# Optimization experiments

Hardware: AMD Instinct MI355X
Metric: run time of the kernel (lower is better)

Reference implementation:

```python
import jax, jax.numpy as jnp
import numpy as np

GE = 8            # graph_embedding_size
AGG_MEAN = 0.0    # undefined global in source; dataset statistic, fixed here
AGG_VAR = 1.0
N_NODES = 100000
N_EDGES = 3200000


def setup_inputs() -> dict:
    key = jax.random.key(0)
    ks = jax.random.split(key, 17)

    def w(k, shape):
        fan_in = shape[0]
        return jax.random.normal(k, shape, jnp.float32) / np.float32(np.sqrt(fan_in))

    x = jax.random.normal(ks[0], (N_NODES, 1 + GE), jnp.float32)
    edge_attr = jax.random.uniform(ks[1], (N_EDGES, 1), dtype=jnp.float32)
    edge_index = jax.random.randint(ks[2], (2, N_EDGES), 0, N_NODES, dtype=jnp.int32)

    # mlp1: Lin(9,32)+ReLU, Lin(32,32)+ReLU, Lin(32,1)+Sigmoid
    W1, b1 = w(ks[3], (1 + GE, 32)), jnp.zeros((32,), jnp.float32)
    W2, b2 = w(ks[4], (32, 32)), jnp.zeros((32,), jnp.float32)
    W3, b3 = w(ks[5], (32, 1)), jnp.zeros((1,), jnp.float32)
    # mlp2: Lin(10,16)+ReLU, Lin(16,8)+ReLU
    V1, c1 = w(ks[6], (2 + GE, 16)), jnp.zeros((16,), jnp.float32)
    V2, c2 = w(ks[7], (16, GE)), jnp.zeros((GE,), jnp.float32)
    # h2o: Lin(8,16)+ReLU, Lin(16,1)+Sigmoid
    H1, d1 = w(ks[8], (GE, 16)), jnp.zeros((16,), jnp.float32)
    H2, d2 = w(ks[9], (16, 1)), jnp.zeros((1,), jnp.float32)

    return {"x": x, "edge_attr": edge_attr, "edge_index": edge_index,
            "W1": W1, "b1": b1, "W2": W2, "b2": b2, "W3": W3, "b3": b3,
            "V1": V1, "c1": c1, "V2": V2, "c2": c2,
            "H1": H1, "d1": d1, "H2": H2, "d2": d2}


def reference(x, edge_attr, edge_index, W1, b1, W2, b2, W3, b3,
              V1, c1, V2, c2, H1, d1, H2, d2):
    src = edge_index[0]  # x_j gathered from source nodes (PyG default flow)
    dst = edge_index[1]  # aggregate into target nodes
    n = x.shape[0]

    def air_conv(xc):
        xj = xc[src]                                            # [E, 9] gather
        h = jax.nn.relu(xj @ W1 + b1)                           # [E, 32]
        h = jax.nn.relu(h @ W2 + b2)                            # [E, 32]
        msg = jax.nn.sigmoid(h @ W3 + b3) * edge_attr           # [E, 1]
        agg = jax.ops.segment_sum(msg, dst, num_segments=n)     # [N, 1] scatter-add
        norm = (agg - AGG_MEAN) / AGG_VAR
        t = jnp.concatenate([xc, norm], axis=1)                 # [N, 10]
        comb = jax.nn.relu(jax.nn.relu(t @ V1 + c1) @ V2 + c2)  # [N, 8]
        return jnp.concatenate([xc[:, :1], comb], axis=1)       # [N, 9]

    out = air_conv(air_conv(air_conv(x)))
    h = jax.nn.relu(out[:, 1:] @ H1 + d1)                       # [N, 16]
    return jax.nn.sigmoid(h @ H2 + d2)                          # [N, 1]
```

## Files before the change

kernel.cpp:

```cpp
#include <hip/hip_runtime.h>

typedef unsigned int uint;
typedef unsigned char uchar;


#define NPB 512
#define NPB_SHIFT 9
#define MAXB 256
#define NBLK 640
#define AGG_THREADS 512

__device__ __forceinline__ void load_smem(float* dstp, const float* __restrict__ srcp,
                                          int n, int tid, int nthreads) {
    for (int i = tid; i < n; i += nthreads) dstp[i] = srcp[i];
}

__device__ __forceinline__ float mlp1_eval(const float* xj,
    const float* sW1, const float* sb1, const float* sW2, const float* sb2,
    const float* sW3, float sb3)
{
    float h1[32];
#pragma unroll
    for (int j = 0; j < 32; ++j) h1[j] = sb1[j];
#pragma unroll
    for (int i = 0; i < 9; ++i) {
        float v = xj[i];
#pragma unroll
        for (int j = 0; j < 32; ++j) h1[j] = fmaf(v, sW1[i*32+j], h1[j]);
    }
#pragma unroll
    for (int j = 0; j < 32; ++j) h1[j] = fmaxf(h1[j], 0.0f);
    float h2[32];
#pragma unroll
    for (int j = 0; j < 32; ++j) h2[j] = sb2[j];
#pragma unroll
    for (int i = 0; i < 32; ++i) {
        float v = h1[i];
#pragma unroll
        for (int j = 0; j < 32; ++j) h2[j] = fmaf(v, sW2[i*32+j], h2[j]);
    }
    float m = sb3;
#pragma unroll
    for (int i = 0; i < 32; ++i) m = fmaf(fmaxf(h2[i], 0.0f), sW3[i], m);
    return 1.0f / (1.0f + __expf(-m));
}

__global__ __launch_bounds__(256) void p0_kernel(
    const float* __restrict__ x,
    const float* __restrict__ W1, const float* __restrict__ b1,
    const float* __restrict__ W2, const float* __restrict__ b2,
    const float* __restrict__ W3, const float* __restrict__ b3,
    float* __restrict__ p, float* __restrict__ agg3, int N)
{
    __shared__ float sW1[288], sb1[32], sW2[1024], sb2[32], sW3[32], sb3s[1];
    int tid = threadIdx.x;
    load_smem(sW1, W1, 288, tid, 256);
    load_smem(sb1, b1, 32, tid, 256);
    load_smem(sW2, W2, 1024, tid, 256);
    load_smem(sb2, b2, 32, tid, 256);
    load_smem(sW3, W3, 32, tid, 256);
    if (tid == 0) sb3s[0] = b3[0];
    __syncthreads();
    int n = blockIdx.x * 256 + tid;
    if (n >= N) return;
    if (agg3) { agg3[n] = 0.0f; agg3[N + n] = 0.0f; agg3[2*(size_t)N + n] = 0.0f; }
    float xj[9];
#pragma unroll
    for (int i = 0; i < 9; ++i) xj[i] = x[(size_t)n*9 + i];
    p[n] = mlp1_eval(xj, sW1, sb1, sW2, sb2, sW3, sb3s[0]);
}


__global__ __launch_bounds__(256) void hist_kernel(
    const int* __restrict__ dst, uint* __restrict__ hist_g, int E, int chunk, int B)
{
    __shared__ uint hist[MAXB];
    int tid = threadIdx.x;
    for (int i = tid; i < MAXB; i += 256) hist[i] = 0u;
    __syncthreads();
    int start = blockIdx.x * chunk;
    int end = min(E, start + chunk);
    for (int e = start + tid; e < end; e += 256)
        atomicAdd(&hist[((uint)dst[e]) >> NPB_SHIFT], 1u);
    __syncthreads();
    for (int b = tid; b < B; b += 256)
        hist_g[(size_t)b * NBLK + blockIdx.x] = hist[b];
}

__global__ __launch_bounds__(1024) void scanA_kernel(
    uint* __restrict__ hist_g, uint* __restrict__ total)
{
    __shared__ uint s[1024];
    int t = threadIdx.x;
    int b = blockIdx.x;
    uint v = (t < NBLK) ? hist_g[(size_t)b * NBLK + t] : 0u;
    s[t] = v;
    __syncthreads();
    for (int off = 1; off < 1024; off <<= 1) {
        uint xv = (t >= off) ? s[t - off] : 0u;
        __syncthreads();
        s[t] += xv;
        __syncthreads();
    }
    if (t < NBLK) hist_g[(size_t)b * NBLK + t] = s[t] - v;
    if (t == NBLK - 1) total[b] = s[t];
}

__global__ __launch_bounds__(1024) void scanB_kernel(
    const uint* __restrict__ total, uint* __restrict__ base, int B)
{
    __shared__ uint s[1024];
    int t = threadIdx.x;
    uint v = (t < B) ? total[t] : 0u;
    s[t] = v;
    __syncthreads();
    for (int off = 1; off < 1024; off <<= 1) {
        uint xv = (t >= off) ? s[t - off] : 0u;
        __syncthreads();
        s[t] += xv;
        __syncthreads();
    }
    if (t < B) base[t] = s[t] - v;
    if (t == B - 1) base[B] = s[t];
}

__global__ __launch_bounds__(256) void scatter_sort_kernel(
    const int* __restrict__ dst, const int* __restrict__ src,
    const float* __restrict__ ea, const uint* __restrict__ base,
    const uint* __restrict__ hist_g,
    int2* __restrict__ ia, int E, int chunk, int B)
{
    __shared__ uint cnt[MAXB];
    int tid = threadIdx.x;
    for (int b = tid; b < B; b += 256)
        cnt[b] = base[b] + hist_g[(size_t)b * NBLK + blockIdx.x];
    __syncthreads();
    int start = blockIdx.x * chunk;
    int end = min(E, start + chunk);
    for (int e = start + tid; e < end; e += 256) {
        uint d = (uint)dst[e];
        uint bin = d >> NPB_SHIFT;
        uint pos = atomicAdd(&cnt[bin], 1u);
        int2 v;
        v.x = (int)(((uint)src[e] << NPB_SHIFT) | (d & (NPB - 1)));
        v.y = __float_as_int(ea[e]);
        ia[pos] = v;
    }
}

template<bool LAST>
__global__ __launch_bounds__(AGG_THREADS) void aggnode_kernel(
    const float* __restrict__ xin,
    const int2* __restrict__ ia,
    const uint* __restrict__ base, const float* __restrict__ p_in,
    const float* __restrict__ V1, const float* __restrict__ c1,
    const float* __restrict__ V2, const float* __restrict__ c2,
    const float* __restrict__ W1, const float* __restrict__ b1,
    const float* __restrict__ W2, const float* __restrict__ b2,
    const float* __restrict__ W3, const float* __restrict__ b3,
    const float* __restrict__ H1, const float* __restrict__ d1,
    const float* __restrict__ H2, const float* __restrict__ d2,
    float* __restrict__ xout, float* __restrict__ pout,
    float* __restrict__ finalout, int N)
{
    __shared__ float aggl[NPB];
    __shared__ float sV1[160], sc1[16], sV2[128], sc2[8];
    __shared__ float sW1[288], sb1[32], sW2[1024], sb2[32], sW3[32], sbx[1];
    __shared__ float sH1[128], sd1[16], sH2[16], sdx[1];
    int tid = threadIdx.x;
    for (int i = tid; i < NPB; i += AGG_THREADS) aggl[i] = 0.0f;
    load_smem(sV1, V1, 160, tid, AGG_THREADS);
    load_smem(sc1, c1, 16, tid, AGG_THREADS);
    load_smem(sV2, V2, 128, tid, AGG_THREADS);
    load_smem(sc2, c2, 8, tid, AGG_THREADS);
    if (!LAST) {
        load_smem(sW1, W1, 288, tid, AGG_THREADS);
        load_smem(sb1, b1, 32, tid, AGG_THREADS);
        load_smem(sW2, W2, 1024, tid, AGG_THREADS);
        load_smem(sb2, b2, 32, tid, AGG_THREADS);
        load_smem(sW3, W3, 32, tid, AGG_THREADS);
        if (tid == 0) sbx[0] = b3[0];
    } else {
        load_smem(sH1, H1, 128, tid, AGG_THREADS);
        load_smem(sd1, d1, 16, tid, AGG_THREADS);
        load_smem(sH2, H2, 16, tid, AGG_THREADS);
        if (tid == 0) sdx[0] = d2[0];
    }
    __syncthreads();

    int b = blockIdx.x;
    uint e0 = base[b], e1 = base[b + 1];
    for (uint e = e0 + tid; e < e1; e += AGG_THREADS) {
        int2 v = ia[e];
        float pv = p_in[(uint)v.x >> NPB_SHIFT];
        atomicAdd(&aggl[(uint)v.x & (NPB - 1)], pv * __int_as_float(v.y));
    }
    __syncthreads();

    int n = b * NPB + tid;
    if (tid >= NPB || n >= N) return;

    float t[10];
#pragma unroll
    for (int i = 0; i < 9; ++i) t[i] = xin[(size_t)n*9 + i];
    t[9] = aggl[tid];

    float u[16];
#pragma unroll
    for (int j = 0; j < 16; ++j) u[j] = sc1[j];
#pragma unroll
    for (int i = 0; i < 10; ++i) {
        float v = t[i];
#pragma unroll
        for (int j = 0; j < 16; ++j) u[j] = fmaf(v, sV1[i*16+j], u[j]);
    }
#pragma unroll
    for (int j = 0; j < 16; ++j) u[j] = fmaxf(u[j], 0.0f);

    float comb[8];
#pragma unroll
    for (int j = 0; j < 8; ++j) comb[j] = sc2[j];
#pragma unroll
    for (int i = 0; i < 16; ++i) {
        float v = u[i];
#pragma unroll
        for (int j = 0; j < 8; ++j) comb[j] = fmaf(v, sV2[i*8+j], comb[j]);
    }
#pragma unroll
    for (int j = 0; j < 8; ++j) comb[j] = fmaxf(comb[j], 0.0f);

    if (!LAST) {
        float xnew[9];
        xnew[0] = t[0];
#pragma unroll
        for (int j = 0; j < 8; ++j) xnew[1+j] = comb[j];
#pragma unroll
        for (int i = 0; i < 9; ++i) xout[(size_t)n*9 + i] = xnew[i];
        pout[n] = mlp1_eval(xnew, sW1, sb1, sW2, sb2, sW3, sbx[0]);
    } else {
        float hh[16];
#pragma unroll
        for (int j = 0; j < 16; ++j) hh[j] = sd1[j];
#pragma unroll
        for (int i = 0; i < 8; ++i) {
            float v = comb[i];
#pragma unroll
            for (int j = 0; j < 16; ++j) hh[j] = fmaf(v, sH1[i*16+j], hh[j]);
        }
        float o = sdx[0];
#pragma unroll
        for (int j = 0; j < 16; ++j) o = fmaf(fmaxf(hh[j], 0.0f), sH2[j], o);
        finalout[n] = 1.0f / (1.0f + __expf(-o));
    }
}


__global__ __launch_bounds__(256) void scatter_kernel4(
    const float* __restrict__ p, const int* __restrict__ src, const int* __restrict__ dst,
    const float* __restrict__ eattr, float* __restrict__ agg, int E)
{
    int i = (blockIdx.x * 256 + threadIdx.x) * 4;
    if (i + 3 < E) {
        int4   s = *(const int4*)(src + i);
        int4   d = *(const int4*)(dst + i);
        float4 a = *(const float4*)(eattr + i);
        atomicAdd(&agg[d.x], p[s.x] * a.x);
        atomicAdd(&agg[d.y], p[s.y] * a.y);
        atomicAdd(&agg[d.z], p[s.z] * a.z);
        atomicAdd(&agg[d.w], p[s.w] * a.w);
    } else {
        for (; i < E; ++i) atomicAdd(&agg[dst[i]], p[src[i]] * eattr[i]);
    }
}

template<bool LAST>
__global__ __launch_bounds__(256) void node_kernel(
    const float* __restrict__ xin, const float* __restrict__ agg,
    const float* __restrict__ V1, const float* __restrict__ c1,
    const float* __restrict__ V2, const float* __restrict__ c2,
    const float* __restrict__ W1, const float* __restrict__ b1,
    const float* __restrict__ W2, const float* __restrict__ b2,
    const float* __restrict__ W3, const float* __restrict__ b3,
    const float* __restrict__ H1, const float* __restrict__ d1,
    const float* __restrict__ H2, const float* __restrict__ d2,
    float* __restrict__ xout, float* __restrict__ pout,
    float* __restrict__ finalout, int N)
{
    __shared__ float sV1[160], sc1[16], sV2[128], sc2[8];
    __shared__ float sW1[288], sb1[32], sW2[1024], sb2[32], sW3[32], sbx[1];
    __shared__ float sH1[128], sd1[16], sH2[16], sdx[1];
    int tid = threadIdx.x;
    load_smem(sV1, V1, 160, tid, 256);
    load_smem(sc1, c1, 16, tid, 256);
    load_smem(sV2, V2, 128, tid, 256);
    load_smem(sc2, c2, 8, tid, 256);
    if (!LAST) {
        load_smem(sW1, W1, 288, tid, 256);
        load_smem(sb1, b1, 32, tid, 256);
        load_smem(sW2, W2, 1024, tid, 256);
        load_smem(sb2, b2, 32, tid, 256);
        load_smem(sW3, W3, 32, tid, 256);
        if (tid == 0) sbx[0] = b3[0];
    } else {
        load_smem(sH1, H1, 128, tid, 256);
        load_smem(sd1, d1, 16, tid, 256);
        load_smem(sH2, H2, 16, tid, 256);
        if (tid == 0) sdx[0] = d2[0];
    }
    __syncthreads();
    int n = blockIdx.x * 256 + tid;
    if (n >= N) return;

    float t[10];
#pragma unroll
    for (int i = 0; i < 9; ++i) t[i] = xin[(size_t)n*9 + i];
    t[9] = agg[n];

    float u[16];
#pragma unroll
    for (int j = 0; j < 16; ++j) u[j] = sc1[j];
#pragma unroll
    for (int i = 0; i < 10; ++i) {
        float v = t[i];
#pragma unroll
        for (int j = 0; j < 16; ++j) u[j] = fmaf(v, sV1[i*16+j], u[j]);
    }
#pragma unroll
    for (int j = 0; j < 16; ++j) u[j] = fmaxf(u[j], 0.0f);

    float comb[8];
#pragma unroll
    for (int j = 0; j < 8; ++j) comb[j] = sc2[j];
#pragma unroll
    for (int i = 0; i < 16; ++i) {
        float v = u[i];
#pragma unroll
        for (int j = 0; j < 8; ++j) comb[j] = fmaf(v, sV2[i*8+j], comb[j]);
    }
#pragma unroll
    for (int j = 0; j < 8; ++j) comb[j] = fmaxf(comb[j], 0.0f);

    if (!LAST) {
        float xnew[9];
        xnew[0] = t[0];
#pragma unroll
        for (int j = 0; j < 8; ++j) xnew[1+j] = comb[j];
#pragma unroll
        for (int i = 0; i < 9; ++i) xout[(size_t)n*9 + i] = xnew[i];
        pout[n] = mlp1_eval(xnew, sW1, sb1, sW2, sb2, sW3, sbx[0]);
    } else {
        float hh[16];
#pragma unroll
        for (int j = 0; j < 16; ++j) hh[j] = sd1[j];
#pragma unroll
        for (int i = 0; i < 8; ++i) {
            float v = comb[i];
#pragma unroll
            for (int j = 0; j < 16; ++j) hh[j] = fmaf(v, sH1[i*16+j], hh[j]);
        }
        float o = sdx[0];
#pragma unroll
        for (int j = 0; j < 16; ++j) o = fmaf(fmaxf(hh[j], 0.0f), sH2[j], o);
        finalout[n] = 1.0f / (1.0f + __expf(-o));
    }
}

extern "C" void kernel_launch(void* const* d_in, const int* in_sizes, int n_in,
                              void* d_out, int out_size, void* d_ws, size_t ws_size,
                              hipStream_t stream)
{
    const float* x     = (const float*)d_in[0];
    const float* eattr = (const float*)d_in[1];
    const int*   eidx  = (const int*)d_in[2];
    const float *W1=(const float*)d_in[3],  *b1=(const float*)d_in[4];
    const float *W2=(const float*)d_in[5],  *b2=(const float*)d_in[6];
    const float *W3=(const float*)d_in[7],  *b3=(const float*)d_in[8];
    const float *V1=(const float*)d_in[9],  *c1=(const float*)d_in[10];
    const float *V2=(const float*)d_in[11], *c2=(const float*)d_in[12];
    const float *H1=(const float*)d_in[13], *d1=(const float*)d_in[14];
    const float *H2=(const float*)d_in[15], *d2=(const float*)d_in[16];
    int N = in_sizes[0] / 9;
    int E = in_sizes[1];
    const int* src = eidx;
    const int* dst = eidx + E;
    float* out = (float*)d_out;
    int B = (N + NPB - 1) / NPB;

    size_t need = (size_t)E * 8
                + (size_t)N * 9 * 4 * 2
                + (size_t)N * 4 * 2
                + (size_t)MAXB * NBLK * 4
                + (size_t)MAXB * 4
                + (size_t)(MAXB + 1) * 4
                + 64;

    dim3 thr(256);
    dim3 blkN((N + 255) / 256);

    bool packable = ((long long)N << NPB_SHIFT) < (1LL << 32);

    if (B <= MAXB && packable && ws_size >= need) {
        char* w = (char*)d_ws;
        int2* ia      = (int2*)w;              w += (size_t)E * 8;
        float* xcA    = (float*)w;             w += (size_t)N * 9 * 4;
        float* xcB    = (float*)w;             w += (size_t)N * 9 * 4;
        float* pA     = (float*)w;             w += (size_t)N * 4;
        float* pB     = (float*)w;             w += (size_t)N * 4;
        uint* hist_g  = (uint*)w;              w += (size_t)MAXB * NBLK * 4;
        uint* total   = (uint*)w;              w += (size_t)MAXB * 4;
        uint* base    = (uint*)w;

        int chunk = (E + NBLK - 1) / NBLK;

        p0_kernel<<<blkN, thr, 0, stream>>>(x, W1,b1,W2,b2,W3,b3, pA, nullptr, N);
        hist_kernel<<<dim3(NBLK), thr, 0, stream>>>(dst, hist_g, E, chunk, B);
        scanA_kernel<<<dim3(B), dim3(1024), 0, stream>>>(hist_g, total);
        scanB_kernel<<<dim3(1), dim3(1024), 0, stream>>>(total, base, B);
        scatter_sort_kernel<<<dim3(NBLK), thr, 0, stream>>>(dst, src, eattr, base, hist_g,
                                                            ia, E, chunk, B);
        aggnode_kernel<false><<<dim3(B), dim3(AGG_THREADS), 0, stream>>>(x, ia, base, pA,
            V1,c1,V2,c2, W1,b1,W2,b2,W3,b3, H1,d1,H2,d2, xcA, pB, nullptr, N);
        aggnode_kernel<false><<<dim3(B), dim3(AGG_THREADS), 0, stream>>>(xcA, ia, base, pB,
            V1,c1,V2,c2, W1,b1,W2,b2,W3,b3, H1,d1,H2,d2, xcB, pA, nullptr, N);
        aggnode_kernel<true><<<dim3(B), dim3(AGG_THREADS), 0, stream>>>(xcB, ia, base, pA,
            V1,c1,V2,c2, W1,b1,W2,b2,W3,b3, H1,d1,H2,d2, nullptr, nullptr, out, N);
    } else {
        float* ws   = (float*)d_ws;
        float* xcA  = ws;
        float* xcB  = xcA + (size_t)N * 9;
        float* p    = xcB + (size_t)N * 9;
        float* agg3 = p + N;
        dim3 blkE4(((E + 3) / 4 + 255) / 256);

        p0_kernel<<<blkN, thr, 0, stream>>>(x, W1,b1,W2,b2,W3,b3, p, agg3, N);
        scatter_kernel4<<<blkE4, thr, 0, stream>>>(p, src, dst, eattr, agg3, E);
        node_kernel<false><<<blkN, thr, 0, stream>>>(x, agg3, V1,c1,V2,c2, W1,b1,W2,b2,W3,b3,
                                                     H1,d1,H2,d2, xcA, p, nullptr, N);
        scatter_kernel4<<<blkE4, thr, 0, stream>>>(p, src, dst, eattr, agg3 + N, E);
        node_kernel<false><<<blkN, thr, 0, stream>>>(xcA, agg3 + N, V1,c1,V2,c2, W1,b1,W2,b2,W3,b3,
                                                     H1,d1,H2,d2, xcB, p, nullptr, N);
        scatter_kernel4<<<blkE4, thr, 0, stream>>>(p, src, dst, eattr, agg3 + 2*(size_t)N, E);
        node_kernel<true><<<blkN, thr, 0, stream>>>(xcB, agg3 + 2*(size_t)N, V1,c1,V2,c2,
                                                    W1,b1,W2,b2,W3,b3, H1,d1,H2,d2,
                                                    nullptr, nullptr, out, N);
    }
}
```

Before: 163.4 us.

## Split edge aggregation across sub-blocks and rebuild bucket sort with local partitioning

Aggregation is separated from the node MLP. Each 512-node bucket is now processed by four blocks that write partial sums, which a separate node kernel adds up; this spreads work across far more blocks than the roughly 196 used before. The per-block histogram and two-level scan are replaced by global atomic bucket counts and a single small scan. The scatter sort becomes a shared-memory local partition per 4096-edge chunk, so global writes are more coalesced. In exchange there are extra kernel launches, a partial-sum buffer round trip, and the node features are updated in place in a buffer marked restrict.

```diff
diff --git a/kernel.cpp b/kernel.cpp
--- a/kernel.cpp
+++ b/kernel.cpp
@@ -1,14 +1,16 @@
 #include <hip/hip_runtime.h>
 
 typedef unsigned int uint;
+typedef unsigned short ushort;
 typedef unsigned char uchar;
 
 
 #define NPB 512
 #define NPB_SHIFT 9
 #define MAXB 256
-#define NBLK 640
-#define AGG_THREADS 512
+#define CHUNK 4096
+#define S_SPLIT 4
+#define NBLK_H 640
 
 __device__ __forceinline__ void load_smem(float* dstp, const float* __restrict__ srcp,
                                           int n, int tid, int nthreads) {
@@ -50,7 +52,7 @@
     const float* __restrict__ W1, const float* __restrict__ b1,
     const float* __restrict__ W2, const float* __restrict__ b2,
     const float* __restrict__ W3, const float* __restrict__ b3,
-    float* __restrict__ p, float* __restrict__ agg3, int N)
+    float* __restrict__ p, uint* __restrict__ count, float* __restrict__ agg3, int N)
 {
     __shared__ float sW1[288], sb1[32], sW2[1024], sb2[32], sW3[32], sb3s[1];
     int tid = threadIdx.x;
@@ -61,6 +63,7 @@
     load_smem(sW3, W3, 32, tid, 256);
     if (tid == 0) sb3s[0] = b3[0];
     __syncthreads();
+    if (count && blockIdx.x == 0) count[tid] = 0u;
     int n = blockIdx.x * 256 + tid;
     if (n >= N) return;
     if (agg3) { agg3[n] = 0.0f; agg3[N + n] = 0.0f; agg3[2*(size_t)N + n] = 0.0f; }
@@ -70,89 +73,129 @@
     p[n] = mlp1_eval(xj, sW1, sb1, sW2, sb2, sW3, sb3s[0]);
 }
 
-
-__global__ __launch_bounds__(256) void hist_kernel(
-    const int* __restrict__ dst, uint* __restrict__ hist_g, int E, int chunk, int B)
+__global__ __launch_bounds__(256) void hist_kernel2(
+    const int* __restrict__ dst, uint* __restrict__ count, int E, int B)
 {
     __shared__ uint hist[MAXB];
     int tid = threadIdx.x;
     for (int i = tid; i < MAXB; i += 256) hist[i] = 0u;
     __syncthreads();
-    int start = blockIdx.x * chunk;
-    int end = min(E, start + chunk);
-    for (int e = start + tid; e < end; e += 256)
+    int total = gridDim.x * 256;
+    int gid = blockIdx.x * 256 + tid;
+    int E4 = E >> 2;
+    const int4* dst4 = (const int4*)dst;
+    for (int i = gid; i < E4; i += total) {
+        int4 d = dst4[i];
+        atomicAdd(&hist[((uint)d.x) >> NPB_SHIFT], 1u);
+        atomicAdd(&hist[((uint)d.y) >> NPB_SHIFT], 1u);
+        atomicAdd(&hist[((uint)d.z) >> NPB_SHIFT], 1u);
+        atomicAdd(&hist[((uint)d.w) >> NPB_SHIFT], 1u);
+    }
+    for (int e = 4*E4 + gid; e < E; e += total)
         atomicAdd(&hist[((uint)dst[e]) >> NPB_SHIFT], 1u);
     __syncthreads();
     for (int b = tid; b < B; b += 256)
-        hist_g[(size_t)b * NBLK + blockIdx.x] = hist[b];
-}
-
-__global__ __launch_bounds__(1024) void scanA_kernel(
-    uint* __restrict__ hist_g, uint* __restrict__ total)
-{
-    __shared__ uint s[1024];
+        if (hist[b]) atomicAdd(&count[b], hist[b]);
+}
+
+__global__ __launch_bounds__(256) void scan_kernel(
+    const uint* __restrict__ count, uint* __restrict__ base,
+    uint* __restrict__ cursor, int B)
+{
+    __shared__ uint s[MAXB];
     int t = threadIdx.x;
-    int b = blockIdx.x;
-    uint v = (t < NBLK) ? hist_g[(size_t)b * NBLK + t] : 0u;
+    uint v = (t < B) ? count[t] : 0u;
     s[t] = v;
     __syncthreads();
-    for (int off = 1; off < 1024; off <<= 1) {
+    for (int off = 1; off < MAXB; off <<= 1) {
         uint xv = (t >= off) ? s[t - off] : 0u;
         __syncthreads();
         s[t] += xv;
         __syncthreads();
     }
-    if (t < NBLK) hist_g[(size_t)b * NBLK + t] = s[t] - v;
-    if (t == NBLK - 1) total[b] = s[t];
-}
-
-__global__ __launch_bounds__(1024) void scanB_kernel(
-    const uint* __restrict__ total, uint* __restrict__ base, int B)
-{
-    __shared__ uint s[1024];
-    int t = threadIdx.x;
-    uint v = (t < B) ? total[t] : 0u;
-    s[t] = v;
-    __syncthreads();
-    for (int off = 1; off < 1024; off <<= 1) {
-        uint xv = (t >= off) ? s[t - off] : 0u;
+    uint excl = s[t] - v;
+    if (t < B) { base[t] = excl; cursor[t] = excl; }
+    if (t == B - 1) base[B] = s[t];
+}
+
+__global__ __launch_bounds__(256) void partition_kernel(
+    const int* __restrict__ dst, const int* __restrict__ src,
+    const float* __restrict__ ea, uint* __restrict__ cursor,
+    int2* __restrict__ ia, int E, int B)
+{
+    __shared__ uint hist[MAXB];
+    __shared__ uint off[MAXB];
+    __shared__ uint gbase[MAXB];
+    __shared__ uchar  sbinA[CHUNK];
+    __shared__ ushort sdloc[CHUNK];
+    __shared__ int2  payload[CHUNK];
+    __shared__ uchar sbin[CHUNK];
+    int tid = threadIdx.x;
+    int start = blockIdx.x * CHUNK;
+    int n = min(E - start, CHUNK);
+    for (int i = tid; i < MAXB; i += 256) hist[i] = 0u;
+    __syncthreads();
+    for (int i = tid; i < n; i += 256) {
+        uint d = (uint)dst[start + i];
+        uint b = d >> NPB_SHIFT;
+        sbinA[i] = (uchar)b;
+        sdloc[i] = (ushort)(d & (NPB - 1));
+        atomicAdd(&hist[b], 1u);
+    }
+    __syncthreads();
+    off[tid] = hist[tid];
+    __syncthreads();
+    for (int o = 1; o < MAXB; o <<= 1) {
+        uint xv = (tid >= o) ? off[tid - o] : 0u;
         __syncthreads();
-        s[t] += xv;
+        off[tid] += xv;
         __syncthreads();
     }
-    if (t < B) base[t] = s[t] - v;
-    if (t == B - 1) base[B] = s[t];
-}
-
-__global__ __launch_bounds__(256) void scatter_sort_kernel(
-    const int* __restrict__ dst, const int* __restrict__ src,
-    const float* __restrict__ ea, const uint* __restrict__ base,
-    const uint* __restrict__ hist_g,
-    int2* __restrict__ ia, int E, int chunk, int B)
-{
-    __shared__ uint cnt[MAXB];
-    int tid = threadIdx.x;
-    for (int b = tid; b < B; b += 256)
-        cnt[b] = base[b] + hist_g[(size_t)b * NBLK + blockIdx.x];
-    __syncthreads();
-    int start = blockIdx.x * chunk;
-    int end = min(E, start + chunk);
-    for (int e = start + tid; e < end; e += 256) {
-        uint d = (uint)dst[e];
-        uint bin = d >> NPB_SHIFT;
-        uint pos = atomicAdd(&cnt[bin], 1u);
+    uint cnt_b = hist[tid];
+    uint excl  = off[tid] - cnt_b;
+    gbase[tid] = cnt_b ? atomicAdd(&cursor[tid], cnt_b) : 0u;
+    off[tid]  = excl;
+    hist[tid] = excl;
+    __syncthreads();
+    for (int i = tid; i < n; i += 256) {
+        uint b = sbinA[i];
+        uint s = atomicAdd(&hist[b], 1u);
         int2 v;
-        v.x = (int)(((uint)src[e] << NPB_SHIFT) | (d & (NPB - 1)));
-        v.y = __float_as_int(ea[e]);
-        ia[pos] = v;
-    }
+        v.x = (int)(((uint)src[start + i] << NPB_SHIFT) | (uint)sdloc[i]);
+        v.y = __float_as_int(ea[start + i]);
+        payload[s] = v;
+        sbin[s] = (uchar)b;
+    }
+    __syncthreads();
+    for (int s2 = tid; s2 < n; s2 += 256) {
+        uint b = sbin[s2];
+        ia[gbase[b] + ((uint)s2 - off[b])] = payload[s2];
+    }
+}
+
+__global__ __launch_bounds__(512) void agg_kernel(
+    const int2* __restrict__ ia, const uint* __restrict__ base,
+    const float* __restrict__ p_in, float* __restrict__ aggpart)
+{
+    __shared__ float aggl[NPB];
+    int tid = threadIdx.x;
+    int bkt = blockIdx.x / S_SPLIT;
+    int sub = blockIdx.x % S_SPLIT;
+    aggl[tid] = 0.0f;
+    __syncthreads();
+    uint e0 = base[bkt], e1 = base[bkt + 1];
+    for (uint e = e0 + (uint)sub * 512u + (uint)tid; e < e1; e += S_SPLIT * 512u) {
+        int2 v = ia[e];
+        atomicAdd(&aggl[(uint)v.x & (NPB - 1)],
+                  p_in[(uint)v.x >> NPB_SHIFT] * __int_as_float(v.y));
+    }
+    __syncthreads();
+    aggpart[(size_t)blockIdx.x * NPB + tid] = aggl[tid];
 }
 
 template<bool LAST>
-__global__ __launch_bounds__(AGG_THREADS) void aggnode_kernel(
-    const float* __restrict__ xin,
-    const int2* __restrict__ ia,
-    const uint* __restrict__ base, const float* __restrict__ p_in,
+__global__ __launch_bounds__(512) void node_kernel2(
+    const float* __restrict__ xin, const float* __restrict__ aggpart,
     const float* __restrict__ V1, const float* __restrict__ c1,
     const float* __restrict__ V2, const float* __restrict__ c2,
     const float* __restrict__ W1, const float* __restrict__ b1,
@@ -163,47 +206,42 @@
     float* __restrict__ xout, float* __restrict__ pout,
     float* __restrict__ finalout, int N)
 {
-    __shared__ float aggl[NPB];
     __shared__ float sV1[160], sc1[16], sV2[128], sc2[8];
     __shared__ float sW1[288], sb1[32], sW2[1024], sb2[32], sW3[32], sbx[1];
     __shared__ float sH1[128], sd1[16], sH2[16], sdx[1];
     int tid = threadIdx.x;
-    for (int i = tid; i < NPB; i += AGG_THREADS) aggl[i] = 0.0f;
-    load_smem(sV1, V1, 160, tid, AGG_THREADS);
-    load_smem(sc1, c1, 16, tid, AGG_THREADS);
-    load_smem(sV2, V2, 128, tid, AGG_THREADS);
-    load_smem(sc2, c2, 8, tid, AGG_THREADS);
+    load_smem(sV1, V1, 160, tid, 512);
+    load_smem(sc1, c1, 16, tid, 512);
+    load_smem(sV2, V2, 128, tid, 512);
+    load_smem(sc2, c2, 8, tid, 512);
     if (!LAST) {
-        load_smem(sW1, W1, 288, tid, AGG_THREADS);
-        load_smem(sb1, b1, 32, tid, AGG_THREADS);
-        load_smem(sW2, W2, 1024, tid, AGG_THREADS);
-        load_smem(sb2, b2, 32, tid, AGG_THREADS);
-        load_smem(sW3, W3, 32, tid, AGG_THREADS);
+        load_smem(sW1, W1, 288, tid, 512);
+        load_smem(sb1, b1, 32, tid, 512);
+        load_smem(sW2, W2, 1024, tid, 512);
+        load_smem(sb2, b2, 32, tid, 512);
+        load_smem(sW3, W3, 32, tid, 512);
         if (tid == 0) sbx[0] = b3[0];
     } else {
-        load_smem(sH1, H1, 128, tid, AGG_THREADS);
-        load_smem(sd1, d1, 16, tid, AGG_THREADS);
-        load_smem(sH2, H2, 16, tid, AGG_THREADS);
+        load_smem(sH1, H1, 128, tid, 512);
+        load_smem(sd1, d1, 16, tid, 512);
+        load_smem(sH2, H2, 16, tid, 512);
         if (tid == 0) sdx[0] = d2[0];
     }
     __syncthreads();
 
-    int b = blockIdx.x;
-    uint e0 = base[b], e1 = base[b + 1];
-    for (uint e = e0 + tid; e < e1; e += AGG_THREADS) {
-        int2 v = ia[e];
-        float pv = p_in[(uint)v.x >> NPB_SHIFT];
-        atomicAdd(&aggl[(uint)v.x & (NPB - 1)], pv * __int_as_float(v.y));
-    }
-    __syncthreads();
-
-    int n = b * NPB + tid;
-    if (tid >= NPB || n >= N) return;
+    int bkt = blockIdx.x;
+    int n = bkt * NPB + tid;
+    if (n >= N) return;
+
+    float aggv = 0.0f;
+#pragma unroll
+    for (int s = 0; s < S_SPLIT; ++s)
+        aggv += aggpart[(size_t)(bkt * S_SPLIT + s) * NPB + tid];
 
     float t[10];
 #pragma unroll
     for (int i = 0; i < 9; ++i) t[i] = xin[(size_t)n*9 + i];
-    t[9] = aggl[tid];
+    t[9] = aggv;
 
     float u[16];
 #pragma unroll
@@ -387,42 +425,43 @@
     int B = (N + NPB - 1) / NPB;
 
     size_t need = (size_t)E * 8
-                + (size_t)N * 9 * 4 * 2
+                + (size_t)N * 9 * 4
                 + (size_t)N * 4 * 2
-                + (size_t)MAXB * NBLK * 4
-                + (size_t)MAXB * 4
-                + (size_t)(MAXB + 1) * 4
-                + 64;
-
-    dim3 thr(256);
+                + (size_t)B * S_SPLIT * NPB * 4
+                + (size_t)MAXB * 4 * 3 + 64;
+
+    dim3 thr256(256), thr512(512);
     dim3 blkN((N + 255) / 256);
-
     bool packable = ((long long)N << NPB_SHIFT) < (1LL << 32);
 
     if (B <= MAXB && packable && ws_size >= need) {
         char* w = (char*)d_ws;
-        int2* ia      = (int2*)w;              w += (size_t)E * 8;
-        float* xcA    = (float*)w;             w += (size_t)N * 9 * 4;
-        float* xcB    = (float*)w;             w += (size_t)N * 9 * 4;
-        float* pA     = (float*)w;             w += (size_t)N * 4;
-        float* pB     = (float*)w;             w += (size_t)N * 4;
-        uint* hist_g  = (uint*)w;              w += (size_t)MAXB * NBLK * 4;
-        uint* total   = (uint*)w;              w += (size_t)MAXB * 4;
-        uint* base    = (uint*)w;
-
-        int chunk = (E + NBLK - 1) / NBLK;
-
-        p0_kernel<<<blkN, thr, 0, stream>>>(x, W1,b1,W2,b2,W3,b3, pA, nullptr, N);
-        hist_kernel<<<dim3(NBLK), thr, 0, stream>>>(dst, hist_g, E, chunk, B);
-        scanA_kernel<<<dim3(B), dim3(1024), 0, stream>>>(hist_g, total);
-        scanB_kernel<<<dim3(1), dim3(1024), 0, stream>>>(total, base, B);
-        scatter_sort_kernel<<<dim3(NBLK), thr, 0, stream>>>(dst, src, eattr, base, hist_g,
-                                                            ia, E, chunk, B);
-        aggnode_kernel<false><<<dim3(B), dim3(AGG_THREADS), 0, stream>>>(x, ia, base, pA,
-            V1,c1,V2,c2, W1,b1,W2,b2,W3,b3, H1,d1,H2,d2, xcA, pB, nullptr, N);
-        aggnode_kernel<false><<<dim3(B), dim3(AGG_THREADS), 0, stream>>>(xcA, ia, base, pB,
-            V1,c1,V2,c2, W1,b1,W2,b2,W3,b3, H1,d1,H2,d2, xcB, pA, nullptr, N);
-        aggnode_kernel<true><<<dim3(B), dim3(AGG_THREADS), 0, stream>>>(xcB, ia, base, pA,
+        int2*  ia      = (int2*)w;   w += (size_t)E * 8;
+        float* xc      = (float*)w;  w += (size_t)N * 9 * 4;
+        float* pA      = (float*)w;  w += (size_t)N * 4;
+        float* pB      = (float*)w;  w += (size_t)N * 4;
+        float* aggpart = (float*)w;  w += (size_t)B * S_SPLIT * NPB * 4;
+        uint*  count   = (uint*)w;   w += (size_t)MAXB * 4;
+        uint*  cursor  = (uint*)w;   w += (size_t)MAXB * 4;
+        uint*  base    = (uint*)w;
+
+        dim3 blkP((E + CHUNK - 1) / CHUNK);
+        dim3 blkA(B * S_SPLIT);
+        dim3 blkB(B);
+
+        p0_kernel<<<blkN, thr256, 0, stream>>>(x, W1,b1,W2,b2,W3,b3, pA, count, nullptr, N);
+        hist_kernel2<<<dim3(NBLK_H), thr256, 0, stream>>>(dst, count, E, B);
+        scan_kernel<<<dim3(1), thr256, 0, stream>>>(count, base, cursor, B);
+        partition_kernel<<<blkP, thr256, 0, stream>>>(dst, src, eattr, cursor, ia, E, B);
+
+        agg_kernel<<<blkA, thr512, 0, stream>>>(ia, base, pA, aggpart);
+        node_kernel2<false><<<blkB, thr512, 0, stream>>>(x, aggpart,
+            V1,c1,V2,c2, W1,b1,W2,b2,W3,b3, H1,d1,H2,d2, xc, pB, nullptr, N);
+        agg_kernel<<<blkA, thr512, 0, stream>>>(ia, base, pB, aggpart);
+        node_kernel2<false><<<blkB, thr512, 0, stream>>>(xc, aggpart,
+            V1,c1,V2,c2, W1,b1,W2,b2,W3,b3, H1,d1,H2,d2, xc, pA, nullptr, N);
+        agg_kernel<<<blkA, thr512, 0, stream>>>(ia, base, pA, aggpart);
+        node_kernel2<true><<<blkB, thr512, 0, stream>>>(xc, aggpart,
             V1,c1,V2,c2, W1,b1,W2,b2,W3,b3, H1,d1,H2,d2, nullptr, nullptr, out, N);
     } else {
         float* ws   = (float*)d_ws;
@@ -432,16 +471,16 @@
         float* agg3 = p + N;
         dim3 blkE4(((E + 3) / 4 + 255) / 256);
 
-        p0_kernel<<<blkN, thr, 0, stream>>>(x, W1,b1,W2,b2,W3,b3, p, agg3, N);
-        scatter_kernel4<<<blkE4, thr, 0, stream>>>(p, src, dst, eattr, agg3, E);
-        node_kernel<false><<<blkN, thr, 0, stream>>>(x, agg3, V1,c1,V2,c2, W1,b1,W2,b2,W3,b3,
-                                                     H1,d1,H2,d2, xcA, p, nullptr, N);
-        scatter_kernel4<<<blkE4, thr, 0, stream>>>(p, src, dst, eattr, agg3 + N, E);
-        node_kernel<false><<<blkN, thr, 0, stream>>>(xcA, agg3 + N, V1,c1,V2,c2, W1,b1,W2,b2,W3,b3,
-                                                     H1,d1,H2,d2, xcB, p, nullptr, N);
-        scatter_kernel4<<<blkE4, thr, 0, stream>>>(p, src, dst, eattr, agg3 + 2*(size_t)N, E);
-        node_kernel<true><<<blkN, thr, 0, stream>>>(xcB, agg3 + 2*(size_t)N, V1,c1,V2,c2,
-                                                    W1,b1,W2,b2,W3,b3, H1,d1,H2,d2,
-                                                    nullptr, nullptr, out, N);
-    }
-}
+        p0_kernel<<<blkN, thr256, 0, stream>>>(x, W1,b1,W2,b2,W3,b3, p, nullptr, agg3, N);
+        scatter_kernel4<<<blkE4, thr256, 0, stream>>>(p, src, dst, eattr, agg3, E);
+        node_kernel<false><<<blkN, thr256, 0, stream>>>(x, agg3, V1,c1,V2,c2, W1,b1,W2,b2,W3,b3,
+                                                        H1,d1,H2,d2, xcA, p, nullptr, N);
+        scatter_kernel4<<<blkE4, thr256, 0, stream>>>(p, src, dst, eattr, agg3 + N, E);
+        node_kernel<false><<<blkN, thr256, 0, stream>>>(xcA, agg3 + N, V1,c1,V2,c2, W1,b1,W2,b2,W3,b3,
+                                                        H1,d1,H2,d2, xcB, p, nullptr, N);
+        scatter_kernel4<<<blkE4, thr256, 0, stream>>>(p, src, dst, eattr, agg3 + 2*(size_t)N, E);
+        node_kernel<true><<<blkN, thr256, 0, stream>>>(xcB, agg3 + 2*(size_t)N, V1,c1,V2,c2,
+                                                       W1,b1,W2,b2,W3,b3, H1,d1,H2,d2,
+                                                       nullptr, nullptr, out, N);
+    }
+}
```

New measurement: 186.3 us. 1.14x slower.
